# Kernel tuning notes

Measured on AMD Instinct MI355X. Metric: run time of the kernel, lower is better.

## Reference

```python
import jax, jax.numpy as jnp
import numpy as np

VOCAB = 1_000_000
EMB = 64
HID = 200
BATCH = 16384
FIELDS = 50
EPS = 1e-5


def batchnorm(x, gamma, beta):
    # training-mode BatchNorm1d: batch statistics, biased variance
    mean = jnp.mean(x, axis=0, keepdims=True)
    var = jnp.var(x, axis=0, keepdims=True)
    return (x - mean) * jax.lax.rsqrt(var + EPS) * gamma + beta


def setup_inputs() -> dict:
    key = jax.random.key(0)
    ks = jax.random.split(key, 9)
    x = jax.random.randint(ks[0], (BATCH, FIELDS), 0, VOCAB)
    emb = jax.random.normal(ks[1], (VOCAB, EMB), dtype=jnp.float32) * 0.01
    w1 = jax.random.normal(ks[2], (EMB, HID), dtype=jnp.float32) * (1.0 / np.sqrt(EMB))
    b1 = jnp.zeros((HID,), dtype=jnp.float32)
    w_last = jax.random.normal(ks[3], (HID, 1), dtype=jnp.float32) * (1.0 / np.sqrt(HID))
    b_last = jnp.zeros((1,), dtype=jnp.float32)
    g_bi = jnp.ones((EMB,), dtype=jnp.float32)
    be_bi = jnp.zeros((EMB,), dtype=jnp.float32)
    g_h = jnp.ones((HID,), dtype=jnp.float32)
    be_h = jnp.zeros((HID,), dtype=jnp.float32)
    return {"x": x, "emb": emb, "w1": w1, "b1": b1, "w_last": w_last,
            "b_last": b_last, "g_bi": g_bi, "be_bi": be_bi, "g_h": g_h, "be_h": be_h}


def reference(x, emb, w1, b1, w_last, b_last, g_bi, be_bi, g_h, be_h):
    e = emb[x]                                # [B, F, E] gather
    # sum_{i<j} e_i * e_j == 0.5 * ((sum e)^2 - sum e^2)  (FM identity)
    s = jnp.sum(e, axis=1)                    # [B, E]
    sq = jnp.sum(e * e, axis=1)               # [B, E]
    bi = 0.5 * (s * s - sq)                   # [B, E]
    h = jax.nn.relu(batchnorm(bi, g_bi, be_bi))
    # single fc layer (layers=1); dropout is identity in eval mode
    h = jax.nn.relu(batchnorm(h @ w1 + b1, g_h, be_h))
    out = jax.nn.sigmoid(h @ w_last + b_last)  # [B, 1]
    return out
```

## Files before the change

### kernel.cpp

```cpp
#include <hip/hip_runtime.h>
#include <hip/hip_bf16.h>

#define BATCH 16384
#define FIELDS 50
#define EMB 64
#define HID 200
#define NCOPY 16

__global__ __launch_bounds__(256) void k_fm(const int* __restrict__ x,
                                            const float* __restrict__ emb,
                                            float* __restrict__ bi,
                                            float* __restrict__ st1) {
    __shared__ int sidx[4][FIELDS];
    __shared__ float sbi[4][EMB];
    const int tid = threadIdx.x;
    const int r = tid >> 6;
    const int d = tid & 63;
    const int b = blockIdx.x * 4 + r;

    if (d < FIELDS) sidx[r][d] = x[b * FIELDS + d];
    __syncthreads();

    float s = 0.f, q = 0.f;
#pragma unroll
    for (int f = 0; f < FIELDS; ++f) {
        float v = emb[(size_t)sidx[r][f] * EMB + d];
        s += v;
        q += v * v;
    }
    float v = 0.5f * (s * s - q);
    bi[b * EMB + d] = v;
    sbi[r][d] = v;
    __syncthreads();

    if (r == 0) {
        float a = 0.f, a2 = 0.f;
#pragma unroll
        for (int i = 0; i < 4; ++i) {
            float t = sbi[i][d];
            a += t;
            a2 += t * t;
        }
        float* st = st1 + (blockIdx.x & (NCOPY - 1)) * 128;
        atomicAdd(st + d, a);
        atomicAdd(st + 64 + d, a2);
    }
}

__global__ void k_fin1(const float* __restrict__ st1,
                       const float* __restrict__ g,
                       const float* __restrict__ be,
                       float* __restrict__ coef) {
    int d = threadIdx.x;
    float s = 0.f, q = 0.f;
    for (int c = 0; c < NCOPY; ++c) {
        s += st1[c * 128 + d];
        q += st1[c * 128 + 64 + d];
    }
    float mean = s * (1.f / BATCH);
    float var = q * (1.f / BATCH) - mean * mean;
    float a = g[d] * rsqrtf(var + 1e-5f);
    coef[d] = a;
    coef[64 + d] = be[d] - mean * a;
}

__global__ __launch_bounds__(256) void k_fc1(const float* __restrict__ bi,
                                             const float* __restrict__ coef,
                                             const float* __restrict__ w1,
                                             const float* __restrict__ b1,
                                             float* __restrict__ y,
                                             float* __restrict__ st2) {
    __shared__ float w1s[EMB * HID + 64];
    __shared__ float b1s[HID];
    const int tid = threadIdx.x;
    for (int i = tid; i < EMB * HID; i += 256) w1s[i] = w1[i];
    if (tid < 64) w1s[EMB * HID + tid] = 0.f;
    if (tid < HID) b1s[tid] = b1[tid];
    __syncthreads();

    const int l = tid & 63;
    const int w = tid >> 6;
    const float a1 = coef[l];
    const float c1v = coef[64 + l];
    const int base_row = blockIdx.x * 32 + w * 8;

    float z[8];
#pragma unroll
    for (int r = 0; r < 8; ++r) {
        float v = bi[(base_row + r) * EMB + l];
        v = a1 * v + c1v;
        z[r] = v > 0.f ? v : 0.f;
    }

    float acc[8][4];
#pragma unroll
    for (int r = 0; r < 8; ++r)
#pragma unroll
        for (int k = 0; k < 4; ++k) acc[r][k] = 0.f;

#pragma unroll 8
    for (int d = 0; d < EMB; ++d) {
        float w0 = w1s[d * HID + l];
        float wv1 = w1s[d * HID + 64 + l];
        float w2 = w1s[d * HID + 128 + l];
        float w3 = w1s[d * HID + 192 + l];
#pragma unroll
        for (int r = 0; r < 8; ++r) {
            float zz = __int_as_float(
                __builtin_amdgcn_readlane(__float_as_int(z[r]), d));
            acc[r][0] += zz * w0;
            acc[r][1] += zz * wv1;
            acc[r][2] += zz * w2;
            acc[r][3] += zz * w3;
        }
    }

    float s0 = 0.f, s1 = 0.f, s2 = 0.f, s3 = 0.f;
    float q0 = 0.f, q1 = 0.f, q2 = 0.f, q3 = 0.f;
    const float bb0 = b1s[l], bb1 = b1s[64 + l], bb2 = b1s[128 + l];
    const float bb3 = (l < 8) ? b1s[192 + l] : 0.f;
#pragma unroll
    for (int r = 0; r < 8; ++r) {
        int row = base_row + r;
        float v0 = acc[r][0] + bb0;
        float v1 = acc[r][1] + bb1;
        float v2 = acc[r][2] + bb2;
        y[row * HID + l] = v0;
        y[row * HID + 64 + l] = v1;
        y[row * HID + 128 + l] = v2;
        s0 += v0; q0 += v0 * v0;
        s1 += v1; q1 += v1 * v1;
        s2 += v2; q2 += v2 * v2;
        if (l < 8) {
            float v3 = acc[r][3] + bb3;
            y[row * HID + 192 + l] = v3;
            s3 += v3; q3 += v3 * v3;
        }
    }
    float* st = st2 + (blockIdx.x & (NCOPY - 1)) * 400;
    atomicAdd(st + l, s0);
    atomicAdd(st + 200 + l, q0);
    atomicAdd(st + 64 + l, s1);
    atomicAdd(st + 200 + 64 + l, q1);
    atomicAdd(st + 128 + l, s2);
    atomicAdd(st + 200 + 128 + l, q2);
    if (l < 8) {
        atomicAdd(st + 192 + l, s3);
        atomicAdd(st + 200 + 192 + l, q3);
    }
}

__global__ void k_fin2(const float* __restrict__ st2,
                       const float* __restrict__ g,
                       const float* __restrict__ be,
                       float* __restrict__ coef) {
    int j = threadIdx.x;
    if (j >= HID) return;
    float s = 0.f, q = 0.f;
    for (int c = 0; c < NCOPY; ++c) {
        s += st2[c * 400 + j];
        q += st2[c * 400 + 200 + j];
    }
    float mean = s * (1.f / BATCH);
    float var = q * (1.f / BATCH) - mean * mean;
    float a = g[j] * rsqrtf(var + 1e-5f);
    coef[j] = a;
    coef[200 + j] = be[j] - mean * a;
}

__global__ __launch_bounds__(256) void k_out(const float* __restrict__ y,
                                             const float* __restrict__ coef,
                                             const float* __restrict__ wl,
                                             const float* __restrict__ bl,
                                             float* __restrict__ out) {
    const int l = threadIdx.x & 63;
    const int w = threadIdx.x >> 6;
    const int j0 = l, j1 = 64 + l, j2 = 128 + l;
    const int j3 = (l < 8) ? (192 + l) : 199;
    const float a0 = coef[j0], c0 = coef[200 + j0];
    const float a1 = coef[j1], c1 = coef[200 + j1];
    const float a2 = coef[j2], c2 = coef[200 + j2];
    const float a3 = coef[j3], c3 = coef[200 + j3];
    const float w0 = wl[j0], w1v = wl[j1], w2 = wl[j2], w3 = wl[j3];
    const float blv = bl[0];

#pragma unroll
    for (int it = 0; it < 4; ++it) {
        int row = blockIdx.x * 16 + it * 4 + w;
        const float* yr = y + row * HID;
        float v0 = a0 * yr[j0] + c0;
        float v1 = a1 * yr[j1] + c1;
        float v2 = a2 * yr[j2] + c2;
        float v3 = a3 * yr[j3] + c3;
        v0 = v0 > 0.f ? v0 : 0.f;
        v1 = v1 > 0.f ? v1 : 0.f;
        v2 = v2 > 0.f ? v2 : 0.f;
        v3 = v3 > 0.f ? v3 : 0.f;
        float t = v0 * w0 + v1 * w1v + v2 * w2 + ((l < 8) ? v3 * w3 : 0.f);
#pragma unroll
        for (int off = 32; off > 0; off >>= 1) t += __shfl_xor(t, off, 64);
        if (l == 0) out[row] = 1.f / (1.f + __expf(-(t + blv)));
    }
}

extern "C" void kernel_launch(void* const* d_in, const int* in_sizes, int n_in,
                              void* d_out, int out_size, void* d_ws, size_t ws_size,
                              hipStream_t stream) {
    const int* x = (const int*)d_in[0];
    const float* emb = (const float*)d_in[1];
    const float* w1 = (const float*)d_in[2];
    const float* b1 = (const float*)d_in[3];
    const float* wl = (const float*)d_in[4];
    const float* bl = (const float*)d_in[5];
    const float* g_bi = (const float*)d_in[6];
    const float* be_bi = (const float*)d_in[7];
    const float* g_h = (const float*)d_in[8];
    const float* be_h = (const float*)d_in[9];
    float* out = (float*)d_out;

    float* ws = (float*)d_ws;
    float* bi = ws;
    float* y = bi + BATCH * EMB;
    float* st1 = y + (size_t)BATCH * HID;
    float* st2 = st1 + NCOPY * 128;
    float* c1 = st2 + NCOPY * 400;
    float* c2 = c1 + 128;

    hipMemsetAsync(st1, 0, (NCOPY * 128 + NCOPY * 400) * sizeof(float), stream);

    k_fm<<<BATCH / 4, 256, 0, stream>>>(x, emb, bi, st1);
    k_fin1<<<1, 64, 0, stream>>>(st1, g_bi, be_bi, c1);
    k_fc1<<<BATCH / 32, 256, 0, stream>>>(bi, c1, w1, b1, y, st2);
    k_fin2<<<1, 256, 0, stream>>>(st2, g_h, be_h, c2);
    k_out<<<BATCH / 16, 256, 0, stream>>>(y, c2, wl, bl, out);
}
```

Before: 70.31 us.

## Fold BN finalize kernels into consumers and vectorize embedding gather with float4

Removes the two single-block finalize kernels by having every block of the consuming kernel recompute the BatchNorm scale/shift from the partial sums into shared memory, cutting two launches and their serialization bubbles. The FM gather kernel now handles 16 rows per block with 16 threads per row loading float4 chunks, and reduces statistics with wave shuffles before one atomic per column per block. This trades redundant small reductions in every block and fewer threads per row for fewer launches and wider memory transactions.

```diff
diff --git a/kernel.cpp b/kernel.cpp
--- a/kernel.cpp
+++ b/kernel.cpp
@@ -11,77 +11,92 @@
                                             const float* __restrict__ emb,
                                             float* __restrict__ bi,
                                             float* __restrict__ st1) {
-    __shared__ int sidx[4][FIELDS];
-    __shared__ float sbi[4][EMB];
+    __shared__ int sidx[16 * FIELDS];
+    __shared__ float swave[4][128];
     const int tid = threadIdx.x;
-    const int r = tid >> 6;
-    const int d = tid & 63;
-    const int b = blockIdx.x * 4 + r;
-
-    if (d < FIELDS) sidx[r][d] = x[b * FIELDS + d];
-    __syncthreads();
-
-    float s = 0.f, q = 0.f;
-#pragma unroll
+    for (int i = tid; i < 16 * FIELDS; i += 256)
+        sidx[i] = x[blockIdx.x * 16 * FIELDS + i];
+    __syncthreads();
+
+    const int r = tid >> 4;
+    const int c = tid & 15;
+    const int* rowidx = sidx + r * FIELDS;
+
+    float s0 = 0.f, s1 = 0.f, s2 = 0.f, s3 = 0.f;
+    float q0 = 0.f, q1 = 0.f, q2 = 0.f, q3 = 0.f;
+#pragma unroll 10
     for (int f = 0; f < FIELDS; ++f) {
-        float v = emb[(size_t)sidx[r][f] * EMB + d];
-        s += v;
-        q += v * v;
-    }
-    float v = 0.5f * (s * s - q);
-    bi[b * EMB + d] = v;
-    sbi[r][d] = v;
-    __syncthreads();
-
-    if (r == 0) {
-        float a = 0.f, a2 = 0.f;
-#pragma unroll
-        for (int i = 0; i < 4; ++i) {
-            float t = sbi[i][d];
-            a += t;
-            a2 += t * t;
-        }
-        float* st = st1 + (blockIdx.x & (NCOPY - 1)) * 128;
-        atomicAdd(st + d, a);
-        atomicAdd(st + 64 + d, a2);
-    }
-}
-
-__global__ void k_fin1(const float* __restrict__ st1,
-                       const float* __restrict__ g,
-                       const float* __restrict__ be,
-                       float* __restrict__ coef) {
-    int d = threadIdx.x;
-    float s = 0.f, q = 0.f;
-    for (int c = 0; c < NCOPY; ++c) {
-        s += st1[c * 128 + d];
-        q += st1[c * 128 + 64 + d];
-    }
-    float mean = s * (1.f / BATCH);
-    float var = q * (1.f / BATCH) - mean * mean;
-    float a = g[d] * rsqrtf(var + 1e-5f);
-    coef[d] = a;
-    coef[64 + d] = be[d] - mean * a;
+        const float4 v = *(const float4*)(emb + (size_t)rowidx[f] * EMB + c * 4);
+        s0 += v.x; q0 += v.x * v.x;
+        s1 += v.y; q1 += v.y * v.y;
+        s2 += v.z; q2 += v.z * v.z;
+        s3 += v.w; q3 += v.w * v.w;
+    }
+    float4 o;
+    o.x = 0.5f * (s0 * s0 - q0);
+    o.y = 0.5f * (s1 * s1 - q1);
+    o.z = 0.5f * (s2 * s2 - q2);
+    o.w = 0.5f * (s3 * s3 - q3);
+    const int row = blockIdx.x * 16 + r;
+    *(float4*)(bi + row * EMB + c * 4) = o;
+
+    float pv0 = o.x, pv1 = o.y, pv2 = o.z, pv3 = o.w;
+    float pq0 = o.x * o.x, pq1 = o.y * o.y, pq2 = o.z * o.z, pq3 = o.w * o.w;
+#pragma unroll
+    for (int off = 16; off <= 32; off <<= 1) {
+        pv0 += __shfl_xor(pv0, off, 64); pq0 += __shfl_xor(pq0, off, 64);
+        pv1 += __shfl_xor(pv1, off, 64); pq1 += __shfl_xor(pq1, off, 64);
+        pv2 += __shfl_xor(pv2, off, 64); pq2 += __shfl_xor(pq2, off, 64);
+        pv3 += __shfl_xor(pv3, off, 64); pq3 += __shfl_xor(pq3, off, 64);
+    }
+    const int lane = tid & 63;
+    const int w = tid >> 6;
+    if (lane < 16) {
+        float4* sv = (float4*)&swave[w][lane * 4];
+        float4* sq = (float4*)&swave[w][64 + lane * 4];
+        *sv = make_float4(pv0, pv1, pv2, pv3);
+        *sq = make_float4(pq0, pq1, pq2, pq3);
+    }
+    __syncthreads();
+    if (tid < 128) {
+        float t = swave[0][tid] + swave[1][tid] + swave[2][tid] + swave[3][tid];
+        atomicAdd(st1 + (blockIdx.x & (NCOPY - 1)) * 128 + tid, t);
+    }
 }
 
 __global__ __launch_bounds__(256) void k_fc1(const float* __restrict__ bi,
-                                             const float* __restrict__ coef,
+                                             const float* __restrict__ st1,
+                                             const float* __restrict__ g_bi,
+                                             const float* __restrict__ be_bi,
                                              const float* __restrict__ w1,
                                              const float* __restrict__ b1,
                                              float* __restrict__ y,
                                              float* __restrict__ st2) {
     __shared__ float w1s[EMB * HID + 64];
     __shared__ float b1s[HID];
+    __shared__ float c1s[128];
     const int tid = threadIdx.x;
     for (int i = tid; i < EMB * HID; i += 256) w1s[i] = w1[i];
     if (tid < 64) w1s[EMB * HID + tid] = 0.f;
     if (tid < HID) b1s[tid] = b1[tid];
+    if (tid < 64) {
+        float s = 0.f, q = 0.f;
+        for (int cc = 0; cc < NCOPY; ++cc) {
+            s += st1[cc * 128 + tid];
+            q += st1[cc * 128 + 64 + tid];
+        }
+        float mean = s * (1.f / BATCH);
+        float var = q * (1.f / BATCH) - mean * mean;
+        float a = g_bi[tid] * rsqrtf(var + 1e-5f);
+        c1s[tid] = a;
+        c1s[64 + tid] = be_bi[tid] - mean * a;
+    }
     __syncthreads();
 
     const int l = tid & 63;
     const int w = tid >> 6;
-    const float a1 = coef[l];
-    const float c1v = coef[64 + l];
+    const float a1 = c1s[l];
+    const float c1v = c1s[64 + l];
     const int base_row = blockIdx.x * 32 + w * 8;
 
     float z[8];
@@ -150,37 +165,37 @@
     }
 }
 
-__global__ void k_fin2(const float* __restrict__ st2,
-                       const float* __restrict__ g,
-                       const float* __restrict__ be,
-                       float* __restrict__ coef) {
-    int j = threadIdx.x;
-    if (j >= HID) return;
-    float s = 0.f, q = 0.f;
-    for (int c = 0; c < NCOPY; ++c) {
-        s += st2[c * 400 + j];
-        q += st2[c * 400 + 200 + j];
-    }
-    float mean = s * (1.f / BATCH);
-    float var = q * (1.f / BATCH) - mean * mean;
-    float a = g[j] * rsqrtf(var + 1e-5f);
-    coef[j] = a;
-    coef[200 + j] = be[j] - mean * a;
-}
-
 __global__ __launch_bounds__(256) void k_out(const float* __restrict__ y,
-                                             const float* __restrict__ coef,
+                                             const float* __restrict__ st2,
+                                             const float* __restrict__ g_h,
+                                             const float* __restrict__ be_h,
                                              const float* __restrict__ wl,
                                              const float* __restrict__ bl,
                                              float* __restrict__ out) {
-    const int l = threadIdx.x & 63;
-    const int w = threadIdx.x >> 6;
+    __shared__ float c2s[400];
+    const int tid = threadIdx.x;
+    if (tid < HID) {
+        float s = 0.f, q = 0.f;
+        for (int cc = 0; cc < NCOPY; ++cc) {
+            s += st2[cc * 400 + tid];
+            q += st2[cc * 400 + 200 + tid];
+        }
+        float mean = s * (1.f / BATCH);
+        float var = q * (1.f / BATCH) - mean * mean;
+        float a = g_h[tid] * rsqrtf(var + 1e-5f);
+        c2s[tid] = a;
+        c2s[200 + tid] = be_h[tid] - mean * a;
+    }
+    __syncthreads();
+
+    const int l = tid & 63;
+    const int w = tid >> 6;
     const int j0 = l, j1 = 64 + l, j2 = 128 + l;
     const int j3 = (l < 8) ? (192 + l) : 199;
-    const float a0 = coef[j0], c0 = coef[200 + j0];
-    const float a1 = coef[j1], c1 = coef[200 + j1];
-    const float a2 = coef[j2], c2 = coef[200 + j2];
-    const float a3 = coef[j3], c3 = coef[200 + j3];
+    const float a0 = c2s[j0], c0 = c2s[200 + j0];
+    const float a1 = c2s[j1], c1 = c2s[200 + j1];
+    const float a2 = c2s[j2], c2 = c2s[200 + j2];
+    const float a3 = c2s[j3], c3 = c2s[200 + j3];
     const float w0 = wl[j0], w1v = wl[j1], w2 = wl[j2], w3 = wl[j3];
     const float blv = bl[0];
 
@@ -223,14 +238,10 @@
     float* y = bi + BATCH * EMB;
     float* st1 = y + (size_t)BATCH * HID;
     float* st2 = st1 + NCOPY * 128;
-    float* c1 = st2 + NCOPY * 400;
-    float* c2 = c1 + 128;
 
     hipMemsetAsync(st1, 0, (NCOPY * 128 + NCOPY * 400) * sizeof(float), stream);
 
-    k_fm<<<BATCH / 4, 256, 0, stream>>>(x, emb, bi, st1);
-    k_fin1<<<1, 64, 0, stream>>>(st1, g_bi, be_bi, c1);
-    k_fc1<<<BATCH / 32, 256, 0, stream>>>(bi, c1, w1, b1, y, st2);
-    k_fin2<<<1, 256, 0, stream>>>(st2, g_h, be_h, c2);
-    k_out<<<BATCH / 16, 256, 0, stream>>>(y, c2, wl, bl, out);
-}
+    k_fm<<<BATCH / 16, 256, 0, stream>>>(x, emb, bi, st1);
+    k_fc1<<<BATCH / 32, 256, 0, stream>>>(bi, st1, g_bi, be_bi, w1, b1, y, st2);
+    k_out<<<BATCH / 16, 256, 0, stream>>>(y, st2, g_h, be_h, wl, bl, out);
+}
```

Measured after the change: 67.67 us. 1.04x faster.
